# Performance work log

Hardware: AMD Instinct MI355X
Metric: run time of the kernel (lower is better)

The kernel has to match this reference:

```python
import jax, jax.numpy as jnp
import numpy as np

N = 100000   # nodes
E = 1200000  # edges
FIN = 128    # in_channels
H = 64       # hidden_channels
OUT = 1      # out_channels


def setup_inputs() -> dict:
    key = jax.random.key(0)
    ks = jax.random.split(key, 12)
    s = 0.05
    return {
        "x": jax.random.normal(ks[0], (N, FIN), jnp.float32),
        "edge_index": jax.random.randint(ks[1], (2, E), 0, N, dtype=jnp.int64),
        "W0": jax.random.normal(ks[2], (FIN, H), jnp.float32) * s,
        "b0": jnp.zeros((H,), jnp.float32),
        "W1": jax.random.normal(ks[3], (H, H), jnp.float32) * s,
        "b1": jnp.zeros((H,), jnp.float32),
        "W2": jax.random.normal(ks[4], (H, OUT), jnp.float32) * s,
        "b2": jnp.zeros((OUT,), jnp.float32),
        "Wm1": jax.random.normal(ks[5], (OUT, H), jnp.float32) * s,
        "bm1": jnp.zeros((H,), jnp.float32),
        "Wm2": jax.random.normal(ks[6], (H, OUT), jnp.float32) * s,
        "bm2": jnp.zeros((OUT,), jnp.float32),
    }


def reference(x, edge_index, W0, b0, W1, b1, W2, b2, Wm1, bm1, Wm2, bm2):
    # GCNConv (PyG default): add self-loops, symmetric normalization D^-1/2 A D^-1/2
    loop = jnp.arange(N, dtype=edge_index.dtype)
    src = jnp.concatenate([edge_index[0], loop])  # [E+N]
    dst = jnp.concatenate([edge_index[1], loop])
    deg = jax.ops.segment_sum(jnp.ones(E + N, jnp.float32), dst, num_segments=N)
    dinv = jax.lax.rsqrt(deg)  # deg >= 1 thanks to self-loops
    norm = dinv[src] * dinv[dst]  # [E+N]

    def conv(h, W, b):
        h = h @ W  # [N, d_out]
        msg = h[src] * norm[:, None]  # gather + scale, [E+N, d_out]
        return jax.ops.segment_sum(msg, dst, num_segments=N) + b

    h = jax.nn.relu(conv(x, W0, b0))   # input layer (dropout is identity in eval)
    h = jax.nn.relu(conv(h, W1, b1))   # hidden layer
    h = conv(h, W2, b2)                # output GCN layer -> [N, OUT]
    # MLP head
    h = jax.nn.relu(h @ Wm1 + bm1) @ Wm2 + bm2
    return h
```

## Files before the change

### kernel.cpp

```cpp
#include <hip/hip_runtime.h>
#include <hip/hip_fp16.h>
#include <math.h>

#define ELL_CAP 48
#define NBUCK 391
#define BCAP 3584

typedef _Float16 half8 __attribute__((ext_vector_type(8)));
typedef float floatx4 __attribute__((ext_vector_type(4)));


__device__ __forceinline__ __half2 u2h(unsigned u) {
  __half2 h; __builtin_memcpy(&h, &u, 4); return h;
}
__device__ __forceinline__ unsigned h2u(__half2 h) {
  unsigned u; __builtin_memcpy(&u, &h, 4); return u;
}


__global__ __launch_bounds__(1024) void k_bucket(const int* __restrict__ src,
                                                 const int* __restrict__ dst,
                                                 int* __restrict__ cursors,
                                                 int* __restrict__ buckets, int E) {
  __shared__ int hist[NBUCK];
  __shared__ int base[NBUCK];
  const int tid = threadIdx.x;
  for (int i = tid; i < NBUCK; i += 1024) hist[i] = 0;
  __syncthreads();

  const long s0 = (long)blockIdx.x * E / gridDim.x;
  const long s1 = (long)(blockIdx.x + 1) * E / gridDim.x;

  for (long e = s0 + tid; e < s1; e += 1024) atomicAdd(&hist[dst[e] >> 8], 1);
  __syncthreads();

  for (int i = tid; i < NBUCK; i += 1024) {
    int c = hist[i];
    base[i] = (c > 0) ? atomicAdd(&cursors[i], c) : 0;
    hist[i] = 0;
  }
  __syncthreads();

  for (long e = s0 + tid; e < s1; e += 1024) {
    int s = src[e], d = dst[e];
    int b = d >> 8;
    int pos = base[b] + atomicAdd(&hist[b], 1);
    if (pos < BCAP) buckets[(long)b * BCAP + pos] = ((d & 255) << 24) | s;
  }
}


__global__ __launch_bounds__(256) void k_ellbuild(const int* __restrict__ buckets,
                                                  const int* __restrict__ cursors,
                                                  int* __restrict__ cnt,
                                                  int* __restrict__ ell,
                                                  float* __restrict__ dinv,
                                                  __half* __restrict__ zrow, int n) {
  __shared__ int cnt_l[256];
  __shared__ int ell_l[256 * ELL_CAP];
  __shared__ unsigned char lim4[256];
  const int b = blockIdx.x, tid = threadIdx.x;
  cnt_l[tid] = 0;
  if (b == 0 && tid < 64) zrow[tid] = __float2half(0.f);
  __syncthreads();

  int m = cursors[b];
  if (m > BCAP) m = BCAP;
  const int* bk = buckets + (long)b * BCAP;
  for (int i = tid; i < m; i += 256) {
    int p = bk[i];
    int ld = ((unsigned)p) >> 24;
    int pos = atomicAdd(&cnt_l[ld], 1);
    if (pos < ELL_CAP) ell_l[ld * ELL_CAP + pos] = p & 0xFFFFFF;
  }
  __syncthreads();

  const int d0 = b << 8;
  const int node = d0 + tid;
  const int rows = min(256, n - d0);
  if (tid < rows) {
    int c = cnt_l[tid];
    if (c > ELL_CAP) c = ELL_CAP;
    cnt[node] = c;
    dinv[node] = 1.0f / sqrtf((float)(c + 1));
    lim4[tid] = (unsigned char)((c + 3) >> 2);
  }
  __syncthreads();

  int4* dst4 = (int4*)(ell + (long)d0 * ELL_CAP);
  const int4* src4 = (const int4*)ell_l;
  const int tot = rows * 12;
  for (int i = tid; i < tot; i += 256) {
    int r = i / 12, w = i - r * 12;
    if (w < (int)lim4[r]) dst4[i] = src4[i];
  }
}


template <int K, bool RELU, bool IN_HALF>
__global__ __launch_bounds__(256) void k_gemm_mfma(const void* __restrict__ Xv,
                                                   const float* __restrict__ W,
                                                   const float* __restrict__ dinv,
                                                   __half* __restrict__ out, int n) {
  constexpr int SP = K + 8;
  constexpr int NS = K / 32;
  __shared__ __half Wl[64 * SP];
  const int tx = threadIdx.x;

  for (int idx = tx; idx < (K / 2) * 64; idx += 256) {
    int k2 = idx >> 6, col = idx & 63;
    __half2 h = __floats2half2_rn(W[(2 * k2) * 64 + col], W[(2 * k2 + 1) * 64 + col]);
    *(__half2*)&Wl[col * SP + 2 * k2] = h;
  }
  __syncthreads();

  const int lane = tx & 63;
  const int l15 = lane & 15;
  const int quad = lane >> 4;
  const long base = (long)blockIdx.x * 64 + (tx >> 6) * 16;

  long arow = base + l15;
  if (arow >= n) arow = n - 1;
  const float* Xf = (const float*)Xv;
  const __half* Xh = (const __half*)Xv;

  half8 afrag[NS];
#pragma unroll
  for (int s = 0; s < NS; ++s) {
    if constexpr (IN_HALF) {
      afrag[s] = *(const half8*)&Xh[arow * K + s * 32 + quad * 8];
    } else {
      float4 lo = *(const float4*)&Xf[arow * K + s * 32 + quad * 8];
      float4 hi = *(const float4*)&Xf[arow * K + s * 32 + quad * 8 + 4];
      half8 a;
      a[0] = (_Float16)lo.x; a[1] = (_Float16)lo.y;
      a[2] = (_Float16)lo.z; a[3] = (_Float16)lo.w;
      a[4] = (_Float16)hi.x; a[5] = (_Float16)hi.y;
      a[6] = (_Float16)hi.z; a[7] = (_Float16)hi.w;
      afrag[s] = a;
    }
    if (RELU) {
      unsigned short* u = (unsigned short*)&afrag[s];
#pragma unroll
      for (int j = 0; j < 8; ++j) u[j] = (u[j] & 0x8000) ? (unsigned short)0 : u[j];
    }
  }

  floatx4 acc[4];
#pragma unroll
  for (int t = 0; t < 4; ++t) acc[t] = (floatx4){0.f, 0.f, 0.f, 0.f};

#pragma unroll
  for (int s = 0; s < NS; ++s) {
#pragma unroll
    for (int t = 0; t < 4; ++t) {
      half8 bfrag = *(const half8*)&Wl[(t * 16 + l15) * SP + s * 32 + quad * 8];
      acc[t] = __builtin_amdgcn_mfma_f32_16x16x32_f16(afrag[s], bfrag, acc[t], 0, 0, 0);
    }
  }

#pragma unroll
  for (int r = 0; r < 4; ++r) {
    long node = base + quad * 4 + r;
    if (node < n) {
      float dv = dinv[node];
#pragma unroll
      for (int t = 0; t < 4; ++t)
        out[node * 64 + t * 16 + l15] = __float2half(acc[t][r] * dv);
    }
  }
}


template <typename EPI>
__device__ __forceinline__ void gather8(const __half* __restrict__ hs,
                                        const int* __restrict__ ell,
                                        const int* __restrict__ cnt,
                                        const float* __restrict__ dinv,
                                        int n, EPI epi) {
  const int tid = threadIdx.x;
  const int lane = tid & 63;
  const int l8 = lane & 7;
  const int wave = (blockIdx.x * 256 + tid) >> 6;
  const int node = wave * 8 + (lane >> 3);
  const bool alive = node < n;
  const int nd = alive ? node : 0;
  const int c = alive ? cnt[nd] : 0;
  const float di = alive ? dinv[nd] : 0.f;
  const int* row = &ell[(long)nd * ELL_CAP];

  int s0 = (l8 < c) ? row[l8] : n;
  int s1 = (8 + l8 < c) ? row[8 + l8] : n;
  int s2 = (16 + l8 < c) ? row[16 + l8] : n;

  int cm = c;
  cm = max(cm, __shfl_xor(cm, 8, 64));
  cm = max(cm, __shfl_xor(cm, 16, 64));
  cm = max(cm, __shfl_xor(cm, 32, 64));
  const int nph = (cm + 7) >> 3;

  float accf[8];
  {
    float4 v = alive ? *(const float4*)&hs[(long)nd * 64 + l8 * 8]
                     : make_float4(0.f, 0.f, 0.f, 0.f);
    const unsigned* up = (const unsigned*)&v;
#pragma unroll
    for (int t = 0; t < 4; ++t) {
      float2 f = __half22float2(u2h(up[t]));
      accf[2 * t] = f.x; accf[2 * t + 1] = f.y;
    }
  }

  auto phase = [&](int reg) {
    int ss[8];
#pragma unroll
    for (int u = 0; u < 8; ++u) ss[u] = __shfl(reg, u, 8);
    float4 vv[8];
#pragma unroll
    for (int u = 0; u < 8; ++u) vv[u] = *(const float4*)&hs[(long)ss[u] * 64 + l8 * 8];
#pragma unroll
    for (int u = 0; u < 8; ++u) {
      const unsigned* up = (const unsigned*)&vv[u];
#pragma unroll
      for (int t = 0; t < 4; ++t) {
        float2 f = __half22float2(u2h(up[t]));
        accf[2 * t] += f.x; accf[2 * t + 1] += f.y;
      }
    }
  };

  if (nph > 0) phase(s0);
  if (nph > 1) phase(s1);
  if (nph > 2) phase(s2);
  for (int ph = 3; ph < nph; ++ph) {
    int reg = (ph * 8 + l8 < c) ? row[ph * 8 + l8] : n;
    phase(reg);
  }

  epi(accf, di, nd, l8, alive);
}

__global__ __launch_bounds__(256) void k_gather64x8(const __half* __restrict__ hs,
                                                    const int* __restrict__ ell,
                                                    const int* __restrict__ cnt,
                                                    const float* __restrict__ dinv,
                                                    const float* __restrict__ b,
                                                    __half* __restrict__ agg, int n) {
  gather8(hs, ell, cnt, dinv, n,
          [&](const float (&accf)[8], float di, int node, int l8, bool alive) {
    if (!alive) return;
    float4 bv0 = *(const float4*)&b[l8 * 8];
    float4 bv1 = *(const float4*)&b[l8 * 8 + 4];
    uint4 o;
    o.x = h2u(__floats2half2_rn(bv0.x + di * accf[0], bv0.y + di * accf[1]));
    o.y = h2u(__floats2half2_rn(bv0.z + di * accf[2], bv0.w + di * accf[3]));
    o.z = h2u(__floats2half2_rn(bv1.x + di * accf[4], bv1.y + di * accf[5]));
    o.w = h2u(__floats2half2_rn(bv1.z + di * accf[6], bv1.w + di * accf[7]));
    *(uint4*)&agg[(long)node * 64 + l8 * 8] = o;
  });
}

__global__ __launch_bounds__(256) void k_gather64x8_dot(const __half* __restrict__ hs,
                                                        const int* __restrict__ ell,
                                                        const int* __restrict__ cnt,
                                                        const float* __restrict__ dinv,
                                                        const float* __restrict__ b1,
                                                        const float* __restrict__ W2,
                                                        float* __restrict__ h2s, int n) {
  if (blockIdx.x == 0 && threadIdx.x == 0) h2s[n] = 0.f;
  gather8(hs, ell, cnt, dinv, n,
          [&](const float (&accf)[8], float di, int node, int l8, bool alive) {
    float4 bv0 = *(const float4*)&b1[l8 * 8];
    float4 bv1 = *(const float4*)&b1[l8 * 8 + 4];
    float4 wv0 = *(const float4*)&W2[l8 * 8];
    float4 wv1 = *(const float4*)&W2[l8 * 8 + 4];
    float part = fmaxf(bv0.x + di * accf[0], 0.f) * wv0.x;
    part = fmaf(fmaxf(bv0.y + di * accf[1], 0.f), wv0.y, part);
    part = fmaf(fmaxf(bv0.z + di * accf[2], 0.f), wv0.z, part);
    part = fmaf(fmaxf(bv0.w + di * accf[3], 0.f), wv0.w, part);
    part = fmaf(fmaxf(bv1.x + di * accf[4], 0.f), wv1.x, part);
    part = fmaf(fmaxf(bv1.y + di * accf[5], 0.f), wv1.y, part);
    part = fmaf(fmaxf(bv1.z + di * accf[6], 0.f), wv1.z, part);
    part = fmaf(fmaxf(bv1.w + di * accf[7], 0.f), wv1.w, part);
#pragma unroll
    for (int off = 1; off < 8; off <<= 1) part += __shfl_xor(part, off, 8);
    if (alive && l8 == 0) h2s[node] = di * part;
  });
}


__global__ __launch_bounds__(256) void k_gather1x8(const float* __restrict__ h2s,
                                                   const int* __restrict__ ell,
                                                   const int* __restrict__ cnt,
                                                   const float* __restrict__ dinv,
                                                   const float* __restrict__ b2,
                                                   float* __restrict__ agg2, int n) {
  const int tid = threadIdx.x;
  const int lane = tid & 63;
  const int l8 = lane & 7;
  const int wave = (blockIdx.x * 256 + tid) >> 6;
  const int node = wave * 8 + (lane >> 3);
  const bool alive = node < n;
  const int nd = alive ? node : 0;
  const int c = alive ? cnt[nd] : 0;
  const float di = alive ? dinv[nd] : 0.f;
  const int* row = &ell[(long)nd * ELL_CAP];

  int cm = c;
  cm = max(cm, __shfl_xor(cm, 8, 64));
  cm = max(cm, __shfl_xor(cm, 16, 64));
  cm = max(cm, __shfl_xor(cm, 32, 64));
  const int nph = (cm + 7) >> 3;

  float acc = (alive && l8 == 0) ? h2s[nd] : 0.f;
  for (int ph = 0; ph < nph; ++ph) {
    int j = ph * 8 + l8;
    int s = (j < c) ? row[j] : n;
    acc += h2s[s];
  }
#pragma unroll
  for (int off = 1; off < 8; off <<= 1) acc += __shfl_xor(acc, off, 8);
  if (alive && l8 == 0) agg2[nd] = b2[0] + di * acc;
}


__global__ void k_mlp(const float* __restrict__ agg2,
                      const float* __restrict__ Wm1, const float* __restrict__ bm1,
                      const float* __restrict__ Wm2, const float* __restrict__ bm2,
                      float* __restrict__ out, int n) {
  __shared__ float w1s[64], w2s[64], b1s[64];
  if (threadIdx.x < 64) {
    w1s[threadIdx.x] = Wm1[threadIdx.x];
    w2s[threadIdx.x] = Wm2[threadIdx.x];
    b1s[threadIdx.x] = bm1[threadIdx.x];
  }
  __syncthreads();
  int i = blockIdx.x * blockDim.x + threadIdx.x;
  if (i >= n) return;
  float s = agg2[i];
  float o = bm2[0];
#pragma unroll
  for (int j = 0; j < 64; ++j)
    o = fmaf(fmaxf(fmaf(s, w1s[j], b1s[j]), 0.f), w2s[j], o);
  out[i] = o;
}


extern "C" void kernel_launch(void* const* d_in, const int* in_sizes, int n_in,
                              void* d_out, int out_size, void* d_ws, size_t ws_size,
                              hipStream_t stream) {
  const float* x   = (const float*)d_in[0];
  const int*   ei  = (const int*)d_in[1];
  const float* W0  = (const float*)d_in[2];
  const float* b0  = (const float*)d_in[3];
  const float* W1  = (const float*)d_in[4];
  const float* b1  = (const float*)d_in[5];
  const float* W2  = (const float*)d_in[6];
  const float* b2  = (const float*)d_in[7];
  const float* Wm1 = (const float*)d_in[8];
  const float* bm1 = (const float*)d_in[9];
  const float* Wm2 = (const float*)d_in[10];
  const float* bm2 = (const float*)d_in[11];

  const int n = in_sizes[0] / 128;
  const int E = in_sizes[1] / 2;
  const int* src = ei;
  const int* dst = ei + E;

  float*  ws   = (float*)d_ws;
  float*  dinv = ws;
  int*    cnt  = (int*)(ws + n);
  int*    ell  = cnt + n;
  __half* bufA = (__half*)(ell + (size_t)n * ELL_CAP);
  __half* bufB = bufA + (size_t)(n + 1) * 64;
  float*  h2s  = (float*)(bufB + (size_t)n * 64);
  float*  agg2 = h2s + (n + 1);
  int*    cursors = (int*)(agg2 + n);
  int*    buckets = (int*)bufA;

  const int nb  = (n + 255) / 256;
  const int g8b = (((n + 7) / 8) + 3) / 4;
  const int mfb = (n + 63) / 64;

  hipMemsetAsync(cursors, 0, NBUCK * sizeof(int), stream);
  k_bucket<<<128, 1024, 0, stream>>>(src, dst, cursors, buckets, E);
  k_ellbuild<<<NBUCK, 256, 0, stream>>>(buckets, cursors, cnt, ell, dinv,
                                        bufA + (size_t)n * 64, n);

  k_gemm_mfma<128, false, false><<<mfb, 256, 0, stream>>>(x, W0, dinv, bufA, n);
  k_gather64x8<<<g8b, 256, 0, stream>>>(bufA, ell, cnt, dinv, b0, bufB, n);

  k_gemm_mfma<64, true, true><<<mfb, 256, 0, stream>>>(bufB, W1, dinv, bufA, n);
  k_gather64x8_dot<<<g8b, 256, 0, stream>>>(bufA, ell, cnt, dinv, b1, W2, h2s, n);

  k_gather1x8<<<g8b, 256, 0, stream>>>(h2s, ell, cnt, dinv, b2, agg2, n);
  k_mlp<<<nb, 256, 0, stream>>>(agg2, Wm1, bm1, Wm2, bm2, (float*)d_out, n);
}
```

Measured before the change: 220.3 us.

## Fuse whole GCN pipeline into one cooperative persistent kernel with grid syncs

```diff
diff --git a/kernel.cpp b/kernel.cpp
--- a/kernel.cpp
+++ b/kernel.cpp
@@ -1,15 +1,18 @@
 #include <hip/hip_runtime.h>
 #include <hip/hip_fp16.h>
+#include <hip/hip_cooperative_groups.h>
 #include <math.h>
+
+namespace cg = cooperative_groups;
 
 #define ELL_CAP 48
 #define NBUCK 391
 #define BCAP 3584
+#define NB 512
 
 typedef _Float16 half8 __attribute__((ext_vector_type(8)));
 typedef float floatx4 __attribute__((ext_vector_type(4)));
 
-
 __device__ __forceinline__ __half2 u2h(unsigned u) {
   __half2 h; __builtin_memcpy(&h, &u, 4); return h;
 }
@@ -17,107 +20,28 @@
   unsigned u; __builtin_memcpy(&u, &h, 4); return u;
 }
 
-
-__global__ __launch_bounds__(1024) void k_bucket(const int* __restrict__ src,
-                                                 const int* __restrict__ dst,
-                                                 int* __restrict__ cursors,
-                                                 int* __restrict__ buckets, int E) {
-  __shared__ int hist[NBUCK];
-  __shared__ int base[NBUCK];
-  const int tid = threadIdx.x;
-  for (int i = tid; i < NBUCK; i += 1024) hist[i] = 0;
-  __syncthreads();
-
-  const long s0 = (long)blockIdx.x * E / gridDim.x;
-  const long s1 = (long)(blockIdx.x + 1) * E / gridDim.x;
-
-  for (long e = s0 + tid; e < s1; e += 1024) atomicAdd(&hist[dst[e] >> 8], 1);
-  __syncthreads();
-
-  for (int i = tid; i < NBUCK; i += 1024) {
-    int c = hist[i];
-    base[i] = (c > 0) ? atomicAdd(&cursors[i], c) : 0;
-    hist[i] = 0;
-  }
-  __syncthreads();
-
-  for (long e = s0 + tid; e < s1; e += 1024) {
-    int s = src[e], d = dst[e];
-    int b = d >> 8;
-    int pos = base[b] + atomicAdd(&hist[b], 1);
-    if (pos < BCAP) buckets[(long)b * BCAP + pos] = ((d & 255) << 24) | s;
-  }
-}
-
-
-__global__ __launch_bounds__(256) void k_ellbuild(const int* __restrict__ buckets,
-                                                  const int* __restrict__ cursors,
-                                                  int* __restrict__ cnt,
-                                                  int* __restrict__ ell,
-                                                  float* __restrict__ dinv,
-                                                  __half* __restrict__ zrow, int n) {
-  __shared__ int cnt_l[256];
-  __shared__ int ell_l[256 * ELL_CAP];
-  __shared__ unsigned char lim4[256];
-  const int b = blockIdx.x, tid = threadIdx.x;
-  cnt_l[tid] = 0;
-  if (b == 0 && tid < 64) zrow[tid] = __float2half(0.f);
-  __syncthreads();
-
-  int m = cursors[b];
-  if (m > BCAP) m = BCAP;
-  const int* bk = buckets + (long)b * BCAP;
-  for (int i = tid; i < m; i += 256) {
-    int p = bk[i];
-    int ld = ((unsigned)p) >> 24;
-    int pos = atomicAdd(&cnt_l[ld], 1);
-    if (pos < ELL_CAP) ell_l[ld * ELL_CAP + pos] = p & 0xFFFFFF;
-  }
-  __syncthreads();
-
-  const int d0 = b << 8;
-  const int node = d0 + tid;
-  const int rows = min(256, n - d0);
-  if (tid < rows) {
-    int c = cnt_l[tid];
-    if (c > ELL_CAP) c = ELL_CAP;
-    cnt[node] = c;
-    dinv[node] = 1.0f / sqrtf((float)(c + 1));
-    lim4[tid] = (unsigned char)((c + 3) >> 2);
-  }
-  __syncthreads();
-
-  int4* dst4 = (int4*)(ell + (long)d0 * ELL_CAP);
-  const int4* src4 = (const int4*)ell_l;
-  const int tot = rows * 12;
-  for (int i = tid; i < tot; i += 256) {
-    int r = i / 12, w = i - r * 12;
-    if (w < (int)lim4[r]) dst4[i] = src4[i];
-  }
-}
+struct P {
+  const float* x; const int* src; const int* dst;
+  const float* W0; const float* b0; const float* W1; const float* b1;
+  const float* W2; const float* b2;
+  const float* Wm1; const float* bm1; const float* Wm2; const float* bm2;
+  float* dinv; int* cnt; int* ell;
+  __half* bufA; __half* bufB;
+  float* h2s; int* cursors; int* buckets;
+  float* out; int n; int E;
+};
 
 
 template <int K, bool RELU, bool IN_HALF>
-__global__ __launch_bounds__(256) void k_gemm_mfma(const void* __restrict__ Xv,
-                                                   const float* __restrict__ W,
-                                                   const float* __restrict__ dinv,
-                                                   __half* __restrict__ out, int n) {
+__device__ __forceinline__ void gemm_tile(long tile, const __half* Wl,
+                                          const void* Xv, const float* dinv,
+                                          __half* out, int n, int tx) {
   constexpr int SP = K + 8;
   constexpr int NS = K / 32;
-  __shared__ __half Wl[64 * SP];
-  const int tx = threadIdx.x;
-
-  for (int idx = tx; idx < (K / 2) * 64; idx += 256) {
-    int k2 = idx >> 6, col = idx & 63;
-    __half2 h = __floats2half2_rn(W[(2 * k2) * 64 + col], W[(2 * k2 + 1) * 64 + col]);
-    *(__half2*)&Wl[col * SP + 2 * k2] = h;
-  }
-  __syncthreads();
-
   const int lane = tx & 63;
   const int l15 = lane & 15;
   const int quad = lane >> 4;
-  const long base = (long)blockIdx.x * 64 + (tx >> 6) * 16;
+  const long base = tile * 64 + (tx >> 6) * 16;
 
   long arow = base + l15;
   if (arow >= n) arow = n - 1;
@@ -173,16 +97,12 @@
 
 
 template <typename EPI>
-__device__ __forceinline__ void gather8(const __half* __restrict__ hs,
-                                        const int* __restrict__ ell,
-                                        const int* __restrict__ cnt,
-                                        const float* __restrict__ dinv,
-                                        int n, EPI epi) {
-  const int tid = threadIdx.x;
-  const int lane = tid & 63;
+__device__ __forceinline__ void gather8_one(int grp, const __half* hs,
+                                            const int* ell, const int* cnt,
+                                            const float* dinv, int n, int lane,
+                                            EPI epi) {
   const int l8 = lane & 7;
-  const int wave = (blockIdx.x * 256 + tid) >> 6;
-  const int node = wave * 8 + (lane >> 3);
+  const int node = grp * 8 + (lane >> 3);
   const bool alive = node < n;
   const int nd = alive ? node : 0;
   const int c = alive ? cnt[nd] : 0;
@@ -240,132 +160,216 @@
   epi(accf, di, nd, l8, alive);
 }
 
-__global__ __launch_bounds__(256) void k_gather64x8(const __half* __restrict__ hs,
-                                                    const int* __restrict__ ell,
-                                                    const int* __restrict__ cnt,
-                                                    const float* __restrict__ dinv,
-                                                    const float* __restrict__ b,
-                                                    __half* __restrict__ agg, int n) {
-  gather8(hs, ell, cnt, dinv, n,
-          [&](const float (&accf)[8], float di, int node, int l8, bool alive) {
-    if (!alive) return;
-    float4 bv0 = *(const float4*)&b[l8 * 8];
-    float4 bv1 = *(const float4*)&b[l8 * 8 + 4];
-    uint4 o;
-    o.x = h2u(__floats2half2_rn(bv0.x + di * accf[0], bv0.y + di * accf[1]));
-    o.y = h2u(__floats2half2_rn(bv0.z + di * accf[2], bv0.w + di * accf[3]));
-    o.z = h2u(__floats2half2_rn(bv1.x + di * accf[4], bv1.y + di * accf[5]));
-    o.w = h2u(__floats2half2_rn(bv1.z + di * accf[6], bv1.w + di * accf[7]));
-    *(uint4*)&agg[(long)node * 64 + l8 * 8] = o;
-  });
-}
-
-__global__ __launch_bounds__(256) void k_gather64x8_dot(const __half* __restrict__ hs,
-                                                        const int* __restrict__ ell,
-                                                        const int* __restrict__ cnt,
-                                                        const float* __restrict__ dinv,
-                                                        const float* __restrict__ b1,
-                                                        const float* __restrict__ W2,
-                                                        float* __restrict__ h2s, int n) {
-  if (blockIdx.x == 0 && threadIdx.x == 0) h2s[n] = 0.f;
-  gather8(hs, ell, cnt, dinv, n,
-          [&](const float (&accf)[8], float di, int node, int l8, bool alive) {
-    float4 bv0 = *(const float4*)&b1[l8 * 8];
-    float4 bv1 = *(const float4*)&b1[l8 * 8 + 4];
-    float4 wv0 = *(const float4*)&W2[l8 * 8];
-    float4 wv1 = *(const float4*)&W2[l8 * 8 + 4];
-    float part = fmaxf(bv0.x + di * accf[0], 0.f) * wv0.x;
-    part = fmaf(fmaxf(bv0.y + di * accf[1], 0.f), wv0.y, part);
-    part = fmaf(fmaxf(bv0.z + di * accf[2], 0.f), wv0.z, part);
-    part = fmaf(fmaxf(bv0.w + di * accf[3], 0.f), wv0.w, part);
-    part = fmaf(fmaxf(bv1.x + di * accf[4], 0.f), wv1.x, part);
-    part = fmaf(fmaxf(bv1.y + di * accf[5], 0.f), wv1.y, part);
-    part = fmaf(fmaxf(bv1.z + di * accf[6], 0.f), wv1.z, part);
-    part = fmaf(fmaxf(bv1.w + di * accf[7], 0.f), wv1.w, part);
-#pragma unroll
-    for (int off = 1; off < 8; off <<= 1) part += __shfl_xor(part, off, 8);
-    if (alive && l8 == 0) h2s[node] = di * part;
-  });
-}
-
-
-__global__ __launch_bounds__(256) void k_gather1x8(const float* __restrict__ h2s,
-                                                   const int* __restrict__ ell,
-                                                   const int* __restrict__ cnt,
-                                                   const float* __restrict__ dinv,
-                                                   const float* __restrict__ b2,
-                                                   float* __restrict__ agg2, int n) {
+
+__global__ __launch_bounds__(256, 2) void k_fused(P p) {
+  cg::grid_group grid = cg::this_grid();
+  __shared__ __align__(16) char smem[50688];
+  const int B = blockIdx.x;
   const int tid = threadIdx.x;
   const int lane = tid & 63;
-  const int l8 = lane & 7;
-  const int wave = (blockIdx.x * 256 + tid) >> 6;
-  const int node = wave * 8 + (lane >> 3);
-  const bool alive = node < n;
-  const int nd = alive ? node : 0;
-  const int c = alive ? cnt[nd] : 0;
-  const float di = alive ? dinv[nd] : 0.f;
-  const int* row = &ell[(long)nd * ELL_CAP];
-
-  int cm = c;
-  cm = max(cm, __shfl_xor(cm, 8, 64));
-  cm = max(cm, __shfl_xor(cm, 16, 64));
-  cm = max(cm, __shfl_xor(cm, 32, 64));
-  const int nph = (cm + 7) >> 3;
-
-  float acc = (alive && l8 == 0) ? h2s[nd] : 0.f;
-  for (int ph = 0; ph < nph; ++ph) {
-    int j = ph * 8 + l8;
-    int s = (j < c) ? row[j] : n;
-    acc += h2s[s];
-  }
-#pragma unroll
-  for (int off = 1; off < 8; off <<= 1) acc += __shfl_xor(acc, off, 8);
-  if (alive && l8 == 0) agg2[nd] = b2[0] + di * acc;
-}
-
-
-__global__ void k_mlp(const float* __restrict__ agg2,
-                      const float* __restrict__ Wm1, const float* __restrict__ bm1,
-                      const float* __restrict__ Wm2, const float* __restrict__ bm2,
-                      float* __restrict__ out, int n) {
-  __shared__ float w1s[64], w2s[64], b1s[64];
-  if (threadIdx.x < 64) {
-    w1s[threadIdx.x] = Wm1[threadIdx.x];
-    w2s[threadIdx.x] = Wm2[threadIdx.x];
-    b1s[threadIdx.x] = bm1[threadIdx.x];
-  }
-  __syncthreads();
-  int i = blockIdx.x * blockDim.x + threadIdx.x;
-  if (i >= n) return;
-  float s = agg2[i];
-  float o = bm2[0];
-#pragma unroll
-  for (int j = 0; j < 64; ++j)
-    o = fmaf(fmaxf(fmaf(s, w1s[j], b1s[j]), 0.f), w2s[j], o);
-  out[i] = o;
+  const int wv = (B * 256 + tid) >> 6;
+  const int nwv = NB * 4;
+  const int n = p.n, E = p.E;
+
+  if (B == 0) {
+    for (int i = tid; i < NBUCK; i += 256) p.cursors[i] = 0;
+  } else if (B == 1) {
+    if (tid < 64) p.bufA[(long)n * 64 + tid] = __float2half(0.f);
+    if (tid == 64) p.h2s[n] = 0.f;
+  }
+  grid.sync();
+
+  {
+    int* hist = (int*)smem;
+    int* base = hist + NBUCK;
+    if (B < 128) {
+      for (int i = tid; i < NBUCK; i += 256) hist[i] = 0;
+      __syncthreads();
+      const long s0 = (long)B * E / 128, s1 = (long)(B + 1) * E / 128;
+      for (long e = s0 + tid; e < s1; e += 256) atomicAdd(&hist[p.dst[e] >> 8], 1);
+      __syncthreads();
+      for (int i = tid; i < NBUCK; i += 256) {
+        int c = hist[i];
+        base[i] = (c > 0) ? atomicAdd(&p.cursors[i], c) : 0;
+        hist[i] = 0;
+      }
+      __syncthreads();
+      for (long e = s0 + tid; e < s1; e += 256) {
+        int s = p.src[e], d = p.dst[e];
+        int b = d >> 8;
+        int pos = base[b] + atomicAdd(&hist[b], 1);
+        if (pos < BCAP) p.buckets[(long)b * BCAP + pos] = ((d & 255) << 24) | s;
+      }
+    }
+  }
+  grid.sync();
+
+  {
+    int* cnt_l = (int*)smem;
+    int* ell_l = cnt_l + 256;
+    unsigned char* lim4 = (unsigned char*)(ell_l + 256 * ELL_CAP);
+    if (B < NBUCK) {
+      cnt_l[tid] = 0;
+      __syncthreads();
+      int m = p.cursors[B];
+      if (m > BCAP) m = BCAP;
+      const int* bk = p.buckets + (long)B * BCAP;
+      for (int i = tid; i < m; i += 256) {
+        int pk = bk[i];
+        int ld = ((unsigned)pk) >> 24;
+        int pos = atomicAdd(&cnt_l[ld], 1);
+        if (pos < ELL_CAP) ell_l[ld * ELL_CAP + pos] = pk & 0xFFFFFF;
+      }
+      __syncthreads();
+      const int d0 = B << 8;
+      const int node = d0 + tid;
+      const int rows = min(256, n - d0);
+      if (tid < rows) {
+        int c = cnt_l[tid];
+        if (c > ELL_CAP) c = ELL_CAP;
+        p.cnt[node] = c;
+        p.dinv[node] = 1.0f / sqrtf((float)(c + 1));
+        lim4[tid] = (unsigned char)((c + 3) >> 2);
+      }
+      __syncthreads();
+      int4* dst4 = (int4*)(p.ell + (long)d0 * ELL_CAP);
+      const int4* src4 = (const int4*)ell_l;
+      const int tot = rows * 12;
+      for (int i = tid; i < tot; i += 256) {
+        int r = i / 12, w = i - r * 12;
+        if (w < (int)lim4[r]) dst4[i] = src4[i];
+      }
+    }
+  }
+  grid.sync();
+
+  {
+    __half* Wl = (__half*)smem;
+    for (int idx = tid; idx < 64 * 64; idx += 256) {
+      int k2 = idx >> 6, col = idx & 63;
+      __half2 h = __floats2half2_rn(p.W0[(2 * k2) * 64 + col],
+                                    p.W0[(2 * k2 + 1) * 64 + col]);
+      *(__half2*)&Wl[col * 136 + 2 * k2] = h;
+    }
+    __syncthreads();
+    const long ntiles = (n + 63) >> 6;
+    for (long t = B; t < ntiles; t += NB)
+      gemm_tile<128, false, false>(t, Wl, p.x, p.dinv, p.bufA, n, tid);
+  }
+  grid.sync();
+
+  {
+    const int groups = (n + 7) >> 3;
+    for (int g = wv; g < groups; g += nwv) {
+      gather8_one(g, p.bufA, p.ell, p.cnt, p.dinv, n, lane,
+                  [&](const float (&accf)[8], float di, int nd, int l8, bool alive) {
+        if (!alive) return;
+        float4 bv0 = *(const float4*)&p.b0[l8 * 8];
+        float4 bv1 = *(const float4*)&p.b0[l8 * 8 + 4];
+        uint4 o;
+        o.x = h2u(__floats2half2_rn(bv0.x + di * accf[0], bv0.y + di * accf[1]));
+        o.y = h2u(__floats2half2_rn(bv0.z + di * accf[2], bv0.w + di * accf[3]));
+        o.z = h2u(__floats2half2_rn(bv1.x + di * accf[4], bv1.y + di * accf[5]));
+        o.w = h2u(__floats2half2_rn(bv1.z + di * accf[6], bv1.w + di * accf[7]));
+        *(uint4*)&p.bufB[(long)nd * 64 + l8 * 8] = o;
+      });
+    }
+  }
+  grid.sync();
+
+  {
+    __half* Wl = (__half*)smem;
+    for (int idx = tid; idx < 32 * 64; idx += 256) {
+      int k2 = idx >> 6, col = idx & 63;
+      __half2 h = __floats2half2_rn(p.W1[(2 * k2) * 64 + col],
+                                    p.W1[(2 * k2 + 1) * 64 + col]);
+      *(__half2*)&Wl[col * 72 + 2 * k2] = h;
+    }
+    __syncthreads();
+    const long ntiles = (n + 63) >> 6;
+    for (long t = B; t < ntiles; t += NB)
+      gemm_tile<64, true, true>(t, Wl, p.bufB, p.dinv, p.bufA, n, tid);
+  }
+  grid.sync();
+
+  {
+    const int groups = (n + 7) >> 3;
+    for (int g = wv; g < groups; g += nwv) {
+      gather8_one(g, p.bufA, p.ell, p.cnt, p.dinv, n, lane,
+                  [&](const float (&accf)[8], float di, int nd, int l8, bool alive) {
+        float4 bv0 = *(const float4*)&p.b1[l8 * 8];
+        float4 bv1 = *(const float4*)&p.b1[l8 * 8 + 4];
+        float4 wv0 = *(const float4*)&p.W2[l8 * 8];
+        float4 wv1 = *(const float4*)&p.W2[l8 * 8 + 4];
+        float part = fmaxf(bv0.x + di * accf[0], 0.f) * wv0.x;
+        part = fmaf(fmaxf(bv0.y + di * accf[1], 0.f), wv0.y, part);
+        part = fmaf(fmaxf(bv0.z + di * accf[2], 0.f), wv0.z, part);
+        part = fmaf(fmaxf(bv0.w + di * accf[3], 0.f), wv0.w, part);
+        part = fmaf(fmaxf(bv1.x + di * accf[4], 0.f), wv1.x, part);
+        part = fmaf(fmaxf(bv1.y + di * accf[5], 0.f), wv1.y, part);
+        part = fmaf(fmaxf(bv1.z + di * accf[6], 0.f), wv1.z, part);
+        part = fmaf(fmaxf(bv1.w + di * accf[7], 0.f), wv1.w, part);
+#pragma unroll
+        for (int off = 1; off < 8; off <<= 1) part += __shfl_xor(part, off, 8);
+        if (alive && l8 == 0) p.h2s[nd] = di * part;
+      });
+    }
+  }
+  grid.sync();
+
+  {
+    float* w1s = (float*)smem;
+    float* w2s = w1s + 64;
+    float* b1s = w2s + 64;
+    if (tid < 64) {
+      w1s[tid] = p.Wm1[tid];
+      w2s[tid] = p.Wm2[tid];
+      b1s[tid] = p.bm1[tid];
+    }
+    __syncthreads();
+    const float b2v = p.b2[0], bm2v = p.bm2[0];
+    const int l8 = lane & 7;
+    const int groups = (n + 7) >> 3;
+    for (int g = wv; g < groups; g += nwv) {
+      const int node = g * 8 + (lane >> 3);
+      const bool alive = node < n;
+      const int nd = alive ? node : 0;
+      const int c = alive ? p.cnt[nd] : 0;
+      const float di = alive ? p.dinv[nd] : 0.f;
+      const int* row = &p.ell[(long)nd * ELL_CAP];
+      int cm = c;
+      cm = max(cm, __shfl_xor(cm, 8, 64));
+      cm = max(cm, __shfl_xor(cm, 16, 64));
+      cm = max(cm, __shfl_xor(cm, 32, 64));
+      const int nph = (cm + 7) >> 3;
+      float acc = (alive && l8 == 0) ? p.h2s[nd] : 0.f;
+      for (int ph = 0; ph < nph; ++ph) {
+        int j = ph * 8 + l8;
+        int s = (j < c) ? row[j] : n;
+        acc += p.h2s[s];
+      }
+#pragma unroll
+      for (int off = 1; off < 8; off <<= 1) acc += __shfl_xor(acc, off, 8);
+      const float sv = b2v + di * acc;
+      float o = 0.f;
+#pragma unroll
+      for (int q = 0; q < 8; ++q) {
+        int j = l8 * 8 + q;
+        o = fmaf(fmaxf(fmaf(sv, w1s[j], b1s[j]), 0.f), w2s[j], o);
+      }
+#pragma unroll
+      for (int off = 1; off < 8; off <<= 1) o += __shfl_xor(o, off, 8);
+      if (alive && l8 == 0) p.out[nd] = o + bm2v;
+    }
+  }
 }
 
 
 extern "C" void kernel_launch(void* const* d_in, const int* in_sizes, int n_in,
                               void* d_out, int out_size, void* d_ws, size_t ws_size,
                               hipStream_t stream) {
-  const float* x   = (const float*)d_in[0];
-  const int*   ei  = (const int*)d_in[1];
-  const float* W0  = (const float*)d_in[2];
-  const float* b0  = (const float*)d_in[3];
-  const float* W1  = (const float*)d_in[4];
-  const float* b1  = (const float*)d_in[5];
-  const float* W2  = (const float*)d_in[6];
-  const float* b2  = (const float*)d_in[7];
-  const float* Wm1 = (const float*)d_in[8];
-  const float* bm1 = (const float*)d_in[9];
-  const float* Wm2 = (const float*)d_in[10];
-  const float* bm2 = (const float*)d_in[11];
-
   const int n = in_sizes[0] / 128;
   const int E = in_sizes[1] / 2;
-  const int* src = ei;
-  const int* dst = ei + E;
 
   float*  ws   = (float*)d_ws;
   float*  dinv = ws;
@@ -374,25 +378,25 @@
   __half* bufA = (__half*)(ell + (size_t)n * ELL_CAP);
   __half* bufB = bufA + (size_t)(n + 1) * 64;
   float*  h2s  = (float*)(bufB + (size_t)n * 64);
-  float*  agg2 = h2s + (n + 1);
-  int*    cursors = (int*)(agg2 + n);
-  int*    buckets = (int*)bufA;
-
-  const int nb  = (n + 255) / 256;
-  const int g8b = (((n + 7) / 8) + 3) / 4;
-  const int mfb = (n + 63) / 64;
-
-  hipMemsetAsync(cursors, 0, NBUCK * sizeof(int), stream);
-  k_bucket<<<128, 1024, 0, stream>>>(src, dst, cursors, buckets, E);
-  k_ellbuild<<<NBUCK, 256, 0, stream>>>(buckets, cursors, cnt, ell, dinv,
-                                        bufA + (size_t)n * 64, n);
-
-  k_gemm_mfma<128, false, false><<<mfb, 256, 0, stream>>>(x, W0, dinv, bufA, n);
-  k_gather64x8<<<g8b, 256, 0, stream>>>(bufA, ell, cnt, dinv, b0, bufB, n);
-
-  k_gemm_mfma<64, true, true><<<mfb, 256, 0, stream>>>(bufB, W1, dinv, bufA, n);
-  k_gather64x8_dot<<<g8b, 256, 0, stream>>>(bufA, ell, cnt, dinv, b1, W2, h2s, n);
-
-  k_gather1x8<<<g8b, 256, 0, stream>>>(h2s, ell, cnt, dinv, b2, agg2, n);
-  k_mlp<<<nb, 256, 0, stream>>>(agg2, Wm1, bm1, Wm2, bm2, (float*)d_out, n);
-}
+  int*    cursors = (int*)(h2s + (n + 1));
+
+  P prm;
+  prm.x   = (const float*)d_in[0];
+  prm.src = (const int*)d_in[1];
+  prm.dst = (const int*)d_in[1] + E;
+  prm.W0  = (const float*)d_in[2];  prm.b0  = (const float*)d_in[3];
+  prm.W1  = (const float*)d_in[4];  prm.b1  = (const float*)d_in[5];
+  prm.W2  = (const float*)d_in[6];  prm.b2  = (const float*)d_in[7];
+  prm.Wm1 = (const float*)d_in[8];  prm.bm1 = (const float*)d_in[9];
+  prm.Wm2 = (const float*)d_in[10]; prm.bm2 = (const float*)d_in[11];
+  prm.dinv = dinv; prm.cnt = cnt; prm.ell = ell;
+  prm.bufA = bufA; prm.bufB = bufB; prm.h2s = h2s;
+  prm.cursors = cursors;
+  prm.buckets = (int*)bufA;
+  prm.out = (float*)d_out;
+  prm.n = n; prm.E = E;
+
+  void* args[] = { &prm };
+  hipLaunchCooperativeKernel((const void*)k_fused, dim3(NB), dim3(256), args, 0,
+                             stream);
+}
```

Result: slower. 654.5 us (+197.1%).
